# Optimization experiments

Hardware: AMD Instinct MI355X
Metric: run time of the kernel (lower is better)

Reference implementation:

```python
import jax, jax.numpy as jnp
import numpy as np

TEMP = 0.1
NEG = -1e30  # stands in for removing the diagonal via masked_select
EPS = 1e-12  # F.normalize eps


def _l2norm(x, axis):
    n = jnp.linalg.norm(x, axis=axis, keepdims=True)
    return x / jnp.maximum(n, EPS)


def setup_inputs() -> dict:
    key = jax.random.key(0)
    k = jax.random.split(key, 6)
    B, D = 8192, 128      # instance batch, embed dim
    Bp, P = 256, 256      # patch batch, patches per sample
    v1_ins = jax.random.normal(k[0], (B, D), jnp.float32)
    v2_ins = jax.random.normal(k[1], (B, D), jnp.float32)
    v1_patch = jax.random.normal(k[2], (Bp, D, P), jnp.float32)
    v2_patch = jax.random.normal(k[3], (Bp, D, P), jnp.float32)
    v1_counts = jax.random.randint(k[4], (Bp, P), 0, 50, dtype=jnp.int32)
    v2_counts = jax.random.randint(k[5], (Bp, P), 0, 50, dtype=jnp.int32)
    return {"v1_ins": v1_ins, "v2_ins": v2_ins,
            "v1_patch": v1_patch, "v2_patch": v2_patch,
            "v1_counts": v1_counts, "v2_counts": v2_counts}


def _instance_ce(v1, v2):
    B = v1.shape[0]
    embs = jnp.concatenate([_l2norm(v1, 1), _l2norm(v2, 1)], axis=0)  # [2B, D]
    logits = (embs @ embs.T) / TEMP                                    # [2B, 2B]
    N = 2 * B
    # masking the diagonal to -inf == masked_select removal; positive of row i
    # is column (i+B) mod 2B (matches labels after diagonal removal shift)
    logits = jnp.where(jnp.eye(N, dtype=bool), NEG, logits)
    labels = jnp.concatenate([jnp.arange(B) + B, jnp.arange(B)])
    logp = jax.nn.log_softmax(logits, axis=1)
    return -jnp.mean(logp[jnp.arange(N), labels])


def _patch_ce(v1, v2, c1, c2):
    Bp, D, P = v1.shape
    embs = jnp.concatenate([_l2norm(v1, 1), _l2norm(v2, 1)], axis=2)   # [Bp, D, 2P]
    logits = jnp.einsum('bdi,bdj->bij', embs, embs) / TEMP             # [Bp, 2P, 2P]
    N = 2 * P
    logits = jnp.where(jnp.eye(N, dtype=bool)[None], NEG, logits)
    labels = jnp.concatenate([jnp.arange(P) + P, jnp.arange(P)])       # [2P]
    valid = ~jnp.concatenate([c1 == 0, c2 == 0], axis=1)               # [Bp, 2P]
    logp = jax.nn.log_softmax(logits, axis=2)
    pos = logp[:, jnp.arange(N), labels]                               # [Bp, 2P]
    # ignore_index=-100 -> mean over non-ignored elements
    n_valid = jnp.sum(valid.astype(logits.dtype))
    return -jnp.sum(jnp.where(valid, pos, 0.0)) / n_valid


def reference(v1_ins, v2_ins, v1_patch, v2_patch, v1_counts, v2_counts):
    ins_ce = _instance_ce(v1_ins, v2_ins)
    patch_ce = _patch_ce(v1_patch, v2_patch, v1_counts, v2_counts)
    return ins_ce + patch_ce
```

## Files before the change

### kernel.cpp

```cpp
#include <hip/hip_runtime.h>
#include <math.h>

typedef __bf16 bf16_t;
typedef __bf16 bf16x8 __attribute__((ext_vector_type(8)));
typedef float f32x4 __attribute__((ext_vector_type(4)));
typedef float f32x2 __attribute__((ext_vector_type(2)));

#define B_INS 8192
#define N_INS 16384
#define D 128
#define BP 256
#define P 256
#define NP 512

#define C1_CONST 14.426950408889634f

#define WS_ACC 0
#define WS_S 8
#define WS_POS (8 + 16384)
#define WS_SP (8 + 2 * 16384)
#define WS_PP (WS_SP + BP * NP)
#define WS_ZERO_FLOATS (WS_PP + BP * NP)
#define EMB_I_BYTE ((((WS_ZERO_FLOATS) * 4 + 15) / 16) * 16)
#define EMB_P_BYTE (EMB_I_BYTE + N_INS * D * 2)


#define NB_NORMI 128
#define NB_NORMP 2048
#define NB_ZERO 289
#define NB_PREP (NB_NORMI + NB_NORMP + NB_ZERO)
#define NB_INS 1088
#define NB_PATCHB 1024
#define NB_GRAM (NB_INS + NB_PATCHB)
#define NB_FIN 576

__device__ __forceinline__ void load_lds16(const bf16_t* g, bf16_t* l) {
    __builtin_amdgcn_global_load_lds(
        (const __attribute__((address_space(1))) void*)g,
        (__attribute__((address_space(3))) void*)l, 16, 0, 0);
}

__device__ __forceinline__ void stage_panel(const bf16_t* __restrict__ src,
                                            bf16_t* dst, int w, int lane) {
    const bf16_t* g = src + w * 4096 + lane * 8;
    bf16_t* d = dst + w * 4096;
#pragma unroll
    for (int it = 0; it < 8; it++)
        load_lds16(g + it * 512, d + it * 512);
}

__device__ __forceinline__ void load_afrags(const bf16_t* __restrict__ abase,
                                            int rh, int tx, int q, bf16x8 af[4][4]) {
    const bf16_t* a = abase + ((rh * 64 + tx) << 3);
#pragma unroll
    for (int rt = 0; rt < 4; rt++)
#pragma unroll
        for (int ks = 0; ks < 4; ks++)
            af[rt][ks] = *(const bf16x8*)(a + (((ks << 2) + q) << 10) + (rt << 7));
}

__global__ __launch_bounds__(256) void prep_k(const float* __restrict__ v1i,
                                              const float* __restrict__ v2i,
                                              const float* __restrict__ v1p,
                                              const float* __restrict__ v2p,
                                              bf16_t* __restrict__ embI,
                                              bf16_t* __restrict__ embP,
                                              float* __restrict__ ws) {
    __shared__ float L[128][65];
    __shared__ float ps[4][64];
    __shared__ float invs[128];
    int bx = blockIdx.x;
    int t = threadIdx.x;
    if (bx < NB_NORMI) {
        int p = bx;
        const float* srcP = (p < 64) ? (v1i + (size_t)p * 128 * D)
                                     : (v2i + (size_t)(p - 64) * 128 * D);
        {
            int r = t >> 1, h = t & 1;
            const float* row = srcP + (size_t)r * D + h * 64;
            float ss = 0.f;
#pragma unroll
            for (int j = 0; j < 16; j++) {
                float4 v = *(const float4*)(row + j * 4);
                ss += v.x * v.x + v.y * v.y + v.z * v.z + v.w * v.w;
            }
            ss += __shfl_xor(ss, 1, 64);
            if (h == 0) invs[r] = 1.0f / fmaxf(sqrtf(ss), 1e-12f);
        }
        __syncthreads();
#pragma unroll
        for (int it = 0; it < 8; it++) {
            int idx = it * 256 + t;
            int r = idx & 127, g = idx >> 7;
            const float* src8 = srcP + (size_t)r * D + g * 8;
            float4 a = *(const float4*)(src8);
            float4 b = *(const float4*)(src8 + 4);
            float inv = invs[r];
            bf16x8 v;
            v[0] = (bf16_t)(a.x * inv); v[1] = (bf16_t)(a.y * inv);
            v[2] = (bf16_t)(a.z * inv); v[3] = (bf16_t)(a.w * inv);
            v[4] = (bf16_t)(b.x * inv); v[5] = (bf16_t)(b.y * inv);
            v[6] = (bf16_t)(b.z * inv); v[7] = (bf16_t)(b.w * inv);
            *(bf16x8*)(embI + ((size_t)p << 14) + (g << 10) + (r << 3)) = v;
        }
    } else if (bx < NB_NORMI + NB_NORMP) {
        int bx2 = bx - NB_NORMI;
        int b = bx2 >> 3, h = (bx2 >> 2) & 1, chunk = bx2 & 3;
        int i0 = chunk * 64;
        const float* src = ((h == 0) ? v1p : v2p) + (size_t)b * D * P;
#pragma unroll
        for (int it = 0; it < 8; it++) {
            int fi = it * 256 + t;
            int d = fi >> 4, c4 = fi & 15;
            float4 v = *(const float4*)(src + (size_t)d * P + i0 + c4 * 4);
            L[d][c4 * 4 + 0] = v.x;
            L[d][c4 * 4 + 1] = v.y;
            L[d][c4 * 4 + 2] = v.z;
            L[d][c4 * 4 + 3] = v.w;
        }
        __syncthreads();
        {
            int col = t & 63, part = t >> 6;
            float ss = 0.f;
#pragma unroll 8
            for (int d = part * 32; d < part * 32 + 32; d++) { float x = L[d][col]; ss += x * x; }
            ps[part][col] = ss;
        }
        __syncthreads();
        if (t < 64) {
            float n2 = ps[0][t] + ps[1][t] + ps[2][t] + ps[3][t];
            invs[t] = 1.0f / fmaxf(sqrtf(n2), 1e-12f);
        }
        __syncthreads();
#pragma unroll
        for (int it = 0; it < 4; it++) {
            int idx = it * 256 + t;
            int ic = idx & 63, g = idx >> 6;
            float inv = invs[ic];
            bf16x8 v;
#pragma unroll
            for (int j = 0; j < 8; j++) v[j] = (bf16_t)(L[g * 8 + j][ic] * inv);
            int iLoc = h * P + i0 + ic;
            *(bf16x8*)(embP + ((size_t)b << 16) + ((size_t)(iLoc >> 7) << 14) +
                       (g << 10) + ((iLoc & 127) << 3)) = v;
        }
    } else {
        int idx = (bx - NB_NORMI - NB_NORMP) * 256 + t;
        if (idx < WS_ZERO_FLOATS / 4)
            ((f32x4*)ws)[idx] = (f32x4){0.f, 0.f, 0.f, 0.f};
    }
}

__global__ __launch_bounds__(256) void gram_k(const bf16_t* __restrict__ embI,
                                              const bf16_t* __restrict__ embP,
                                              float* __restrict__ S,
                                              float* __restrict__ pos,
                                              float* __restrict__ Sp,
                                              float* __restrict__ posp) {
    __shared__ __align__(16) bf16_t shB[2][16384];
    int t = threadIdx.x, w = t >> 6, lane = t & 63;
    int tx = lane & 15, q = lane >> 4;
    int rh = w & 1, ch = w >> 1;
    int bx = blockIdx.x;

    const bf16_t *Abase, *Bbase;
    float *Sarr, *posArr;
    int R, c0, n, diagC, posC;
    if (bx < NB_INS) {
        int bid = bx, k = 0, cum = 0;
        while (bid >= cum + 8 * (16 - k)) { cum += 8 * (16 - k); k++; }
        int rem = bid - cum, cc = 16 - k;
        R = 8 * k + rem / cc;
        int ci = rem - (rem / cc) * cc;
        c0 = R + ci * 8;
        n = min(8, 128 - c0);
        Abase = embI + ((size_t)R << 14);
        Bbase = embI;
        Sarr = S; posArr = pos;
        diagC = R; posC = R + 64;
    } else {
        int pi = bx - NB_INS;
        int b = pi >> 2; R = pi & 3;
        c0 = R; n = 4 - R;
        const bf16_t* base = embP + ((size_t)b << 16);
        Abase = base + ((size_t)R << 14);
        Bbase = base;
        Sarr = Sp + (size_t)b * NP; posArr = posp + (size_t)b * NP;
        diagC = R; posC = R + 2;
    }
    int rowBase = R * 128;

    bf16x8 af[4][4];
    load_afrags(Abase, rh, tx, q, af);

    f32x2 rowS2[8];
#pragma unroll
    for (int i = 0; i < 8; i++) rowS2[i] = (f32x2){0.f, 0.f};

    stage_panel(Bbase + ((size_t)c0 << 14), shB[0], w, lane);
    int cur = 0;
    for (int ti = 0; ti < n; ti++) {
        int C = c0 + ti;
        __syncthreads();
        if (ti + 1 < n)
            stage_panel(Bbase + ((size_t)(C + 1) << 14), shB[cur ^ 1], w, lane);
        bool isDiag = (C == diagC), isPos = (C == posC);
        int colBase = C * 128;
        const bf16_t* sb = shB[cur];

        float colS[4];
#pragma unroll
        for (int nt = 0; nt < 4; nt++) {
            bf16x8 bf[4];
#pragma unroll
            for (int ks = 0; ks < 4; ks++)
                bf[ks] = *(const bf16x8*)(sb + (((ks << 2) + q) << 10) +
                                          ((ch * 64 + nt * 16 + tx) << 3));
            f32x4 acc[4];
#pragma unroll
            for (int rt = 0; rt < 4; rt++) acc[rt] = (f32x4){0.f, 0.f, 0.f, 0.f};
#pragma unroll
            for (int ks = 0; ks < 4; ks++)
#pragma unroll
                for (int rt = 0; rt < 4; rt++)
                    acc[rt] = __builtin_amdgcn_mfma_f32_16x16x32_bf16(
                        af[rt][ks], bf[ks], acc[rt], 0, 0, 0);

            f32x2 cs = (f32x2){0.f, 0.f};
#pragma unroll
            for (int rt = 0; rt < 4; rt++) {
                f32x2 l0 = {acc[rt][0], acc[rt][1]};
                f32x2 l1 = {acc[rt][2], acc[rt][3]};
                l0 = l0 * C1_CONST - C1_CONST;
                l1 = l1 * C1_CONST - C1_CONST;
                f32x2 e0 = {__builtin_amdgcn_exp2f(l0.x), __builtin_amdgcn_exp2f(l0.y)};
                f32x2 e1 = {__builtin_amdgcn_exp2f(l1.x), __builtin_amdgcn_exp2f(l1.y)};
                if (isDiag) {
                    int inRow = rh * 64 + rt * 16 + q * 4;
                    int inCol = ch * 64 + nt * 16 + tx;
                    if (inRow + 0 == inCol) e0.x = 0.f;
                    if (inRow + 1 == inCol) e0.y = 0.f;
                    if (inRow + 2 == inCol) e1.x = 0.f;
                    if (inRow + 3 == inCol) e1.y = 0.f;
                }
                rowS2[rt * 2] += e0;
                rowS2[rt * 2 + 1] += e1;
                cs += e0 + e1;
            }
            colS[nt] = cs.x + cs.y;

            if (isPos && ch == rh) {
                int reg = tx - q * 4;
                if (reg >= 0 && reg < 4) {
                    float pl = acc[nt][reg] * 10.0f;
                    atomicAdd(&posArr[rowBase + rh * 64 + nt * 16 + tx], pl);
                    atomicAdd(&posArr[colBase + rh * 64 + nt * 16 + tx], pl);
                }
            }
        }
        if (!isDiag) {
#pragma unroll
            for (int i = 0; i < 4; i++) {
                colS[i] += __shfl_xor(colS[i], 16, 64);
                colS[i] += __shfl_xor(colS[i], 32, 64);
            }
            if (q == 0) {
#pragma unroll
                for (int nt = 0; nt < 4; nt++)
                    atomicAdd(&Sarr[colBase + ch * 64 + nt * 16 + tx], colS[nt]);
            }
        }
        cur ^= 1;
    }
    float* rowS = (float*)rowS2;
#pragma unroll
    for (int off = 1; off <= 8; off <<= 1)
#pragma unroll
        for (int i = 0; i < 16; i++) rowS[i] += __shfl_xor(rowS[i], off, 16);
    if (tx == 0) {
#pragma unroll
        for (int rt = 0; rt < 4; rt++)
#pragma unroll
            for (int reg = 0; reg < 4; reg++)
                atomicAdd(&Sarr[rowBase + rh * 64 + rt * 16 + q * 4 + reg],
                          rowS[rt * 4 + reg]);
    }
}

__global__ __launch_bounds__(256) void fin_k(const float* __restrict__ S,
                                             const float* __restrict__ pos,
                                             const float* __restrict__ Sp,
                                             const float* __restrict__ posp,
                                             const int* __restrict__ c1,
                                             const int* __restrict__ c2,
                                             float* __restrict__ acc,
                                             float* __restrict__ out) {
    int bx = blockIdx.x, t = threadIdx.x;
    int lane = t & 63, w = t >> 6;
    float va = 0.f, nv = 0.f;
    if (bx < 64) {
        int i = bx * 256 + t;
        va = __logf(S[i]) + 10.0f - pos[i];
    } else {
        int idx = (bx - 64) * 256 + t;
        int b = idx >> 9, i = idx & 511;
        int cnt = (i < P) ? c1[b * P + i] : c2[b * P + i - P];
        bool valid = (cnt != 0);
        va = valid ? (__logf(Sp[idx]) + 10.0f - posp[idx]) : 0.f;
        nv = valid ? 1.0f : 0.0f;
    }
#pragma unroll
    for (int off = 32; off >= 1; off >>= 1) {
        va += __shfl_down(va, off, 64);
        nv += __shfl_down(nv, off, 64);
    }
    __shared__ float ps[4], pn[4];
    if (lane == 0) { ps[w] = va; pn[w] = nv; }
    __syncthreads();
    if (t == 0) {
        float sv = ps[0] + ps[1] + ps[2] + ps[3];
        float sn = pn[0] + pn[1] + pn[2] + pn[3];
        if (bx < 64) {
            atomicAdd(&acc[0], sv);
        } else {
            atomicAdd(&acc[1], sv);
            atomicAdd(&acc[2], sn);
        }
        __threadfence();
        unsigned old = atomicAdd((unsigned*)&acc[3], 1u);
        if (old == NB_FIN - 1) {
            float a0 = atomicAdd(&acc[0], 0.0f);
            float a1 = atomicAdd(&acc[1], 0.0f);
            float a2 = atomicAdd(&acc[2], 0.0f);
            out[0] = a0 * (1.0f / (float)N_INS) + a1 / a2;
        }
    }
}

extern "C" void kernel_launch(void* const* d_in, const int* in_sizes, int n_in,
                              void* d_out, int out_size, void* d_ws, size_t ws_size,
                              hipStream_t stream) {
    const float* v1i = (const float*)d_in[0];
    const float* v2i = (const float*)d_in[1];
    const float* v1p = (const float*)d_in[2];
    const float* v2p = (const float*)d_in[3];
    const int* c1 = (const int*)d_in[4];
    const int* c2 = (const int*)d_in[5];
    float* ws = (float*)d_ws;
    float* out = (float*)d_out;
    bf16_t* embI = (bf16_t*)((char*)d_ws + EMB_I_BYTE);
    bf16_t* embP = (bf16_t*)((char*)d_ws + EMB_P_BYTE);

    prep_k<<<NB_PREP, 256, 0, stream>>>(v1i, v2i, v1p, v2p, embI, embP, ws);
    gram_k<<<NB_GRAM, 256, 0, stream>>>(embI, embP, ws + WS_S, ws + WS_POS,
                                        ws + WS_SP, ws + WS_PP);
    fin_k<<<NB_FIN, 256, 0, stream>>>(ws + WS_S, ws + WS_POS, ws + WS_SP,
                                      ws + WS_PP, c1, c2, ws + WS_ACC, out);
}
```

Measured before the change: 221.9 us.

## Stage half-width 64-column B panels in gram kernel and parallelize instance normalization

The gram kernel now stages 64-column halves of each B panel, so the double buffer in LDS shrinks to half its size and the pipeline runs twice as many smaller iterations. Diagonal, positive-pair and column-sum indexing are remapped to the 64-column granularity. Separately, instance-row normalization now uses 256 blocks with four threads per row, each holding its 32 floats in registers, which removes the second pass over global memory. The smaller LDS footprint may raise occupancy, at the cost of more barriers and more column atomics per row tile.

After: 232.2 us. 4.7% more time.

```diff
diff --git a/kernel.cpp b/kernel.cpp
--- a/kernel.cpp
+++ b/kernel.cpp
@@ -25,7 +25,7 @@
 #define EMB_P_BYTE (EMB_I_BYTE + N_INS * D * 2)
 
 
-#define NB_NORMI 128
+#define NB_NORMI 256
 #define NB_NORMP 2048
 #define NB_ZERO 289
 #define NB_PREP (NB_NORMI + NB_NORMP + NB_ZERO)
@@ -40,13 +40,14 @@
         (__attribute__((address_space(3))) void*)l, 16, 0, 0);
 }
 
-__device__ __forceinline__ void stage_panel(const bf16_t* __restrict__ src,
-                                            bf16_t* dst, int w, int lane) {
-    const bf16_t* g = src + w * 4096 + lane * 8;
-    bf16_t* d = dst + w * 4096;
-#pragma unroll
-    for (int it = 0; it < 8; it++)
-        load_lds16(g + it * 512, d + it * 512);
+__device__ __forceinline__ void stage_half(const bf16_t* __restrict__ panel,
+                                           int c0loc, bf16_t* dst, int w, int lane) {
+    const bf16_t* g = panel + ((c0loc + lane) << 3);
+#pragma unroll
+    for (int it = 0; it < 4; it++) {
+        int gi = w * 4 + it;
+        load_lds16(g + (gi << 10), dst + (gi << 9));
+    }
 }
 
 __device__ __forceinline__ void load_afrags(const bf16_t* __restrict__ abase,
@@ -68,40 +69,34 @@
                                               float* __restrict__ ws) {
     __shared__ float L[128][65];
     __shared__ float ps[4][64];
-    __shared__ float invs[128];
+    __shared__ float invs[64];
     int bx = blockIdx.x;
     int t = threadIdx.x;
     if (bx < NB_NORMI) {
-        int p = bx;
-        const float* srcP = (p < 64) ? (v1i + (size_t)p * 128 * D)
-                                     : (v2i + (size_t)(p - 64) * 128 * D);
-        {
-            int r = t >> 1, h = t & 1;
-            const float* row = srcP + (size_t)r * D + h * 64;
-            float ss = 0.f;
-#pragma unroll
-            for (int j = 0; j < 16; j++) {
-                float4 v = *(const float4*)(row + j * 4);
-                ss += v.x * v.x + v.y * v.y + v.z * v.z + v.w * v.w;
-            }
-            ss += __shfl_xor(ss, 1, 64);
-            if (h == 0) invs[r] = 1.0f / fmaxf(sqrtf(ss), 1e-12f);
-        }
-        __syncthreads();
-#pragma unroll
-        for (int it = 0; it < 8; it++) {
-            int idx = it * 256 + t;
-            int r = idx & 127, g = idx >> 7;
-            const float* src8 = srcP + (size_t)r * D + g * 8;
-            float4 a = *(const float4*)(src8);
-            float4 b = *(const float4*)(src8 + 4);
-            float inv = invs[r];
+        int r = t >> 2, h = t & 3;
+        int i = bx * 64 + r;
+        const float* row = ((i < B_INS) ? (v1i + (size_t)i * D)
+                                        : (v2i + (size_t)(i - B_INS) * D)) + h * 32;
+        float4 f[8];
+#pragma unroll
+        for (int j = 0; j < 8; j++) f[j] = *(const float4*)(row + j * 4);
+        float ss = 0.f;
+#pragma unroll
+        for (int j = 0; j < 8; j++)
+            ss += f[j].x * f[j].x + f[j].y * f[j].y + f[j].z * f[j].z + f[j].w * f[j].w;
+        ss += __shfl_xor(ss, 1, 64);
+        ss += __shfl_xor(ss, 2, 64);
+        float inv = 1.0f / fmaxf(sqrtf(ss), 1e-12f);
+        int p = i >> 7, rl = i & 127;
+#pragma unroll
+        for (int j = 0; j < 4; j++) {
+            float4 a = f[2 * j], b = f[2 * j + 1];
             bf16x8 v;
             v[0] = (bf16_t)(a.x * inv); v[1] = (bf16_t)(a.y * inv);
             v[2] = (bf16_t)(a.z * inv); v[3] = (bf16_t)(a.w * inv);
             v[4] = (bf16_t)(b.x * inv); v[5] = (bf16_t)(b.y * inv);
             v[6] = (bf16_t)(b.z * inv); v[7] = (bf16_t)(b.w * inv);
-            *(bf16x8*)(embI + ((size_t)p << 14) + (g << 10) + (r << 3)) = v;
+            *(bf16x8*)(embI + ((size_t)p << 14) + ((h * 4 + j) << 10) + (rl << 3)) = v;
         }
     } else if (bx < NB_NORMI + NB_NORMP) {
         int bx2 = bx - NB_NORMI;
@@ -157,36 +152,36 @@
                                               float* __restrict__ pos,
                                               float* __restrict__ Sp,
                                               float* __restrict__ posp) {
-    __shared__ __align__(16) bf16_t shB[2][16384];
+    __shared__ __align__(16) bf16_t shB[2][8192];
     int t = threadIdx.x, w = t >> 6, lane = t & 63;
     int tx = lane & 15, q = lane >> 4;
-    int rh = w & 1, ch = w >> 1;
+    int rh = w & 1, cq = w >> 1;
     int bx = blockIdx.x;
 
     const bf16_t *Abase, *Bbase;
     float *Sarr, *posArr;
-    int R, c0, n, diagC, posC;
+    int R, c0, n, diag0, pos0;
     if (bx < NB_INS) {
         int bid = bx, k = 0, cum = 0;
         while (bid >= cum + 8 * (16 - k)) { cum += 8 * (16 - k); k++; }
         int rem = bid - cum, cc = 16 - k;
         R = 8 * k + rem / cc;
         int ci = rem - (rem / cc) * cc;
-        c0 = R + ci * 8;
-        n = min(8, 128 - c0);
+        c0 = 2 * R + ci * 16;
+        n = min(16, 256 - c0);
         Abase = embI + ((size_t)R << 14);
         Bbase = embI;
         Sarr = S; posArr = pos;
-        diagC = R; posC = R + 64;
+        diag0 = 2 * R; pos0 = 2 * R + 128;
     } else {
         int pi = bx - NB_INS;
         int b = pi >> 2; R = pi & 3;
-        c0 = R; n = 4 - R;
+        c0 = 2 * R; n = 8 - 2 * R;
         const bf16_t* base = embP + ((size_t)b << 16);
         Abase = base + ((size_t)R << 14);
         Bbase = base;
         Sarr = Sp + (size_t)b * NP; posArr = posp + (size_t)b * NP;
-        diagC = R; posC = R + 2;
+        diag0 = 2 * R; pos0 = 2 * R + 4;
     }
     int rowBase = R * 128;
 
@@ -197,25 +192,30 @@
 #pragma unroll
     for (int i = 0; i < 8; i++) rowS2[i] = (f32x2){0.f, 0.f};
 
-    stage_panel(Bbase + ((size_t)c0 << 14), shB[0], w, lane);
+    stage_half(Bbase + ((size_t)(c0 >> 1) << 14), (c0 & 1) * 64, shB[0], w, lane);
     int cur = 0;
     for (int ti = 0; ti < n; ti++) {
-        int C = c0 + ti;
+        int C64 = c0 + ti;
         __syncthreads();
-        if (ti + 1 < n)
-            stage_panel(Bbase + ((size_t)(C + 1) << 14), shB[cur ^ 1], w, lane);
-        bool isDiag = (C == diagC), isPos = (C == posC);
-        int colBase = C * 128;
+        if (ti + 1 < n) {
+            int nc = C64 + 1;
+            stage_half(Bbase + ((size_t)(nc >> 1) << 14), (nc & 1) * 64,
+                       shB[cur ^ 1], w, lane);
+        }
+        int h = C64 & 1;
+        bool isDiag = ((C64 & ~1) == diag0);
+        bool isPos = ((C64 & ~1) == pos0);
+        int colBase = C64 * 64;
         const bf16_t* sb = shB[cur];
 
-        float colS[4];
-#pragma unroll
-        for (int nt = 0; nt < 4; nt++) {
+        float colS[2];
+#pragma unroll
+        for (int nt = 0; nt < 2; nt++) {
+            int cloc = cq * 32 + nt * 16 + tx;
             bf16x8 bf[4];
 #pragma unroll
             for (int ks = 0; ks < 4; ks++)
-                bf[ks] = *(const bf16x8*)(sb + (((ks << 2) + q) << 10) +
-                                          ((ch * 64 + nt * 16 + tx) << 3));
+                bf[ks] = *(const bf16x8*)(sb + (((ks << 2) + q) << 9) + (cloc << 3));
             f32x4 acc[4];
 #pragma unroll
             for (int rt = 0; rt < 4; rt++) acc[rt] = (f32x4){0.f, 0.f, 0.f, 0.f};
@@ -235,13 +235,12 @@
                 l1 = l1 * C1_CONST - C1_CONST;
                 f32x2 e0 = {__builtin_amdgcn_exp2f(l0.x), __builtin_amdgcn_exp2f(l0.y)};
                 f32x2 e1 = {__builtin_amdgcn_exp2f(l1.x), __builtin_amdgcn_exp2f(l1.y)};
-                if (isDiag) {
-                    int inRow = rh * 64 + rt * 16 + q * 4;
-                    int inCol = ch * 64 + nt * 16 + tx;
-                    if (inRow + 0 == inCol) e0.x = 0.f;
-                    if (inRow + 1 == inCol) e0.y = 0.f;
-                    if (inRow + 2 == inCol) e1.x = 0.f;
-                    if (inRow + 3 == inCol) e1.y = 0.f;
+                if (isDiag && rh == h) {
+                    int inRow = rt * 16 + q * 4;
+                    if (inRow + 0 == cloc) e0.x = 0.f;
+                    if (inRow + 1 == cloc) e0.y = 0.f;
+                    if (inRow + 2 == cloc) e1.x = 0.f;
+                    if (inRow + 3 == cloc) e1.y = 0.f;
                 }
                 rowS2[rt * 2] += e0;
                 rowS2[rt * 2 + 1] += e1;
@@ -249,25 +248,26 @@
             }
             colS[nt] = cs.x + cs.y;
 
-            if (isPos && ch == rh) {
+            if (isPos && rh == h) {
                 int reg = tx - q * 4;
                 if (reg >= 0 && reg < 4) {
-                    float pl = acc[nt][reg] * 10.0f;
-                    atomicAdd(&posArr[rowBase + rh * 64 + nt * 16 + tx], pl);
-                    atomicAdd(&posArr[colBase + rh * 64 + nt * 16 + tx], pl);
+                    int rt_m = cq * 2 + nt;
+                    float pl = acc[rt_m][reg] * 10.0f;
+                    atomicAdd(&posArr[rowBase + rh * 64 + rt_m * 16 + tx], pl);
+                    atomicAdd(&posArr[colBase + cloc], pl);
                 }
             }
         }
         if (!isDiag) {
 #pragma unroll
-            for (int i = 0; i < 4; i++) {
+            for (int i = 0; i < 2; i++) {
                 colS[i] += __shfl_xor(colS[i], 16, 64);
                 colS[i] += __shfl_xor(colS[i], 32, 64);
             }
             if (q == 0) {
 #pragma unroll
-                for (int nt = 0; nt < 4; nt++)
-                    atomicAdd(&Sarr[colBase + ch * 64 + nt * 16 + tx], colS[nt]);
+                for (int nt = 0; nt < 2; nt++)
+                    atomicAdd(&Sarr[colBase + cq * 32 + nt * 16 + tx], colS[nt]);
             }
         }
         cur ^= 1;
```

## Load Gram B-fragments directly from global into registers, drop LDS staging

Applied to the files above, without the earlier changes.

The Gram kernel no longer stages 128-column B panels into shared memory with global_load_lds and per-panel barriers. Each wave now loads its B fragments straight from global memory into two register buffers, prefetching two steps ahead. The instance strip length shrinks from 8 to 4 panels, roughly doubling the number of instance blocks for more parallelism. The instance normalization is also reworked so one quad of threads owns a row and keeps it in registers, over twice as many blocks. The aim is to remove LDS traffic and sync overhead, at the cost of redundant global or L2 reads across waves and more atomics from the extra strips.

After: 247.9 us. +11.7%, slower.

```diff
diff --git a/kernel.cpp b/kernel.cpp
--- a/kernel.cpp
+++ b/kernel.cpp
@@ -25,29 +25,14 @@
 #define EMB_P_BYTE (EMB_I_BYTE + N_INS * D * 2)
 
 
-#define NB_NORMI 128
+#define NB_NORMI 256
 #define NB_NORMP 2048
 #define NB_ZERO 289
 #define NB_PREP (NB_NORMI + NB_NORMP + NB_ZERO)
-#define NB_INS 1088
+#define NB_INS 2112
 #define NB_PATCHB 1024
 #define NB_GRAM (NB_INS + NB_PATCHB)
 #define NB_FIN 576
-
-__device__ __forceinline__ void load_lds16(const bf16_t* g, bf16_t* l) {
-    __builtin_amdgcn_global_load_lds(
-        (const __attribute__((address_space(1))) void*)g,
-        (__attribute__((address_space(3))) void*)l, 16, 0, 0);
-}
-
-__device__ __forceinline__ void stage_panel(const bf16_t* __restrict__ src,
-                                            bf16_t* dst, int w, int lane) {
-    const bf16_t* g = src + w * 4096 + lane * 8;
-    bf16_t* d = dst + w * 4096;
-#pragma unroll
-    for (int it = 0; it < 8; it++)
-        load_lds16(g + it * 512, d + it * 512);
-}
 
 __device__ __forceinline__ void load_afrags(const bf16_t* __restrict__ abase,
                                             int rh, int tx, int q, bf16x8 af[4][4]) {
@@ -68,40 +53,34 @@
                                               float* __restrict__ ws) {
     __shared__ float L[128][65];
     __shared__ float ps[4][64];
-    __shared__ float invs[128];
+    __shared__ float invs[64];
     int bx = blockIdx.x;
     int t = threadIdx.x;
     if (bx < NB_NORMI) {
-        int p = bx;
-        const float* srcP = (p < 64) ? (v1i + (size_t)p * 128 * D)
-                                     : (v2i + (size_t)(p - 64) * 128 * D);
-        {
-            int r = t >> 1, h = t & 1;
-            const float* row = srcP + (size_t)r * D + h * 64;
-            float ss = 0.f;
-#pragma unroll
-            for (int j = 0; j < 16; j++) {
-                float4 v = *(const float4*)(row + j * 4);
-                ss += v.x * v.x + v.y * v.y + v.z * v.z + v.w * v.w;
-            }
-            ss += __shfl_xor(ss, 1, 64);
-            if (h == 0) invs[r] = 1.0f / fmaxf(sqrtf(ss), 1e-12f);
-        }
-        __syncthreads();
-#pragma unroll
-        for (int it = 0; it < 8; it++) {
-            int idx = it * 256 + t;
-            int r = idx & 127, g = idx >> 7;
-            const float* src8 = srcP + (size_t)r * D + g * 8;
-            float4 a = *(const float4*)(src8);
-            float4 b = *(const float4*)(src8 + 4);
-            float inv = invs[r];
+        int r = t >> 2, h = t & 3;
+        int i = bx * 64 + r;
+        const float* row = ((i < B_INS) ? (v1i + (size_t)i * D)
+                                        : (v2i + (size_t)(i - B_INS) * D)) + h * 32;
+        float4 f[8];
+#pragma unroll
+        for (int j = 0; j < 8; j++) f[j] = *(const float4*)(row + j * 4);
+        float ss = 0.f;
+#pragma unroll
+        for (int j = 0; j < 8; j++)
+            ss += f[j].x * f[j].x + f[j].y * f[j].y + f[j].z * f[j].z + f[j].w * f[j].w;
+        ss += __shfl_xor(ss, 1, 64);
+        ss += __shfl_xor(ss, 2, 64);
+        float inv = 1.0f / fmaxf(sqrtf(ss), 1e-12f);
+        int p = i >> 7, rl = i & 127;
+#pragma unroll
+        for (int j = 0; j < 4; j++) {
+            float4 a = f[2 * j], b = f[2 * j + 1];
             bf16x8 v;
             v[0] = (bf16_t)(a.x * inv); v[1] = (bf16_t)(a.y * inv);
             v[2] = (bf16_t)(a.z * inv); v[3] = (bf16_t)(a.w * inv);
             v[4] = (bf16_t)(b.x * inv); v[5] = (bf16_t)(b.y * inv);
             v[6] = (bf16_t)(b.z * inv); v[7] = (bf16_t)(b.w * inv);
-            *(bf16x8*)(embI + ((size_t)p << 14) + (g << 10) + (r << 3)) = v;
+            *(bf16x8*)(embI + ((size_t)p << 14) + ((h * 4 + j) << 10) + (rl << 3)) = v;
         }
     } else if (bx < NB_NORMI + NB_NORMP) {
         int bx2 = bx - NB_NORMI;
@@ -151,13 +130,83 @@
     }
 }
 
+__device__ __forceinline__ void gram_step(int it, int itn, int c0, int coff,
+                                          const bf16_t* __restrict__ Bbase,
+                                          bf16x8 (&bufC)[4],
+                                          const bf16x8 (&af)[4][4],
+                                          int diagC, int posC, int rowBase,
+                                          int rh, int ch, int tx, int q,
+                                          f32x2 (&rowS2)[8],
+                                          float* __restrict__ Sarr,
+                                          float* __restrict__ posArr) {
+    int ti = it >> 2, nt = it & 3;
+    int C = c0 + ti;
+    bool isDiag = (C == diagC), isPos = (C == posC);
+    int colBase = C * 128;
+
+    f32x4 acc[4];
+#pragma unroll
+    for (int rt = 0; rt < 4; rt++) acc[rt] = (f32x4){0.f, 0.f, 0.f, 0.f};
+#pragma unroll
+    for (int ks = 0; ks < 4; ks++)
+#pragma unroll
+        for (int rt = 0; rt < 4; rt++)
+            acc[rt] = __builtin_amdgcn_mfma_f32_16x16x32_bf16(
+                af[rt][ks], bufC[ks], acc[rt], 0, 0, 0);
+
+    if (it + 2 < itn) {
+        int i2 = it + 2;
+        const bf16_t* bb = Bbase + ((size_t)(c0 + (i2 >> 2)) << 14) + coff +
+                           ((i2 & 3) << 7);
+#pragma unroll
+        for (int ks = 0; ks < 4; ks++)
+            bufC[ks] = *(const bf16x8*)(bb + (((ks << 2) + q) << 10));
+    }
+
+    f32x2 cs = (f32x2){0.f, 0.f};
+#pragma unroll
+    for (int rt = 0; rt < 4; rt++) {
+        f32x2 l0 = {acc[rt][0], acc[rt][1]};
+        f32x2 l1 = {acc[rt][2], acc[rt][3]};
+        l0 = l0 * C1_CONST - C1_CONST;
+        l1 = l1 * C1_CONST - C1_CONST;
+        f32x2 e0 = {__builtin_amdgcn_exp2f(l0.x), __builtin_amdgcn_exp2f(l0.y)};
+        f32x2 e1 = {__builtin_amdgcn_exp2f(l1.x), __builtin_amdgcn_exp2f(l1.y)};
+        if (isDiag) {
+            int inRow = rh * 64 + rt * 16 + q * 4;
+            int inCol = ch * 64 + nt * 16 + tx;
+            if (inRow + 0 == inCol) e0.x = 0.f;
+            if (inRow + 1 == inCol) e0.y = 0.f;
+            if (inRow + 2 == inCol) e1.x = 0.f;
+            if (inRow + 3 == inCol) e1.y = 0.f;
+        }
+        rowS2[rt * 2] += e0;
+        rowS2[rt * 2 + 1] += e1;
+        cs += e0 + e1;
+    }
+    float colS = cs.x + cs.y;
+    if (!isDiag) {
+        colS += __shfl_xor(colS, 16, 64);
+        colS += __shfl_xor(colS, 32, 64);
+        if (q == 0)
+            atomicAdd(&Sarr[colBase + ch * 64 + nt * 16 + tx], colS);
+    }
+    if (isPos && ch == rh) {
+        int reg = tx - q * 4;
+        if (reg >= 0 && reg < 4) {
+            float pl = acc[nt][reg] * 10.0f;
+            atomicAdd(&posArr[rowBase + rh * 64 + nt * 16 + tx], pl);
+            atomicAdd(&posArr[colBase + ch * 64 + nt * 16 + tx], pl);
+        }
+    }
+}
+
 __global__ __launch_bounds__(256) void gram_k(const bf16_t* __restrict__ embI,
                                               const bf16_t* __restrict__ embP,
                                               float* __restrict__ S,
                                               float* __restrict__ pos,
                                               float* __restrict__ Sp,
                                               float* __restrict__ posp) {
-    __shared__ __align__(16) bf16_t shB[2][16384];
     int t = threadIdx.x, w = t >> 6, lane = t & 63;
     int tx = lane & 15, q = lane >> 4;
     int rh = w & 1, ch = w >> 1;
@@ -168,12 +217,12 @@
     int R, c0, n, diagC, posC;
     if (bx < NB_INS) {
         int bid = bx, k = 0, cum = 0;
-        while (bid >= cum + 8 * (16 - k)) { cum += 8 * (16 - k); k++; }
-        int rem = bid - cum, cc = 16 - k;
-        R = 8 * k + rem / cc;
+        while (bid >= cum + 4 * (32 - k)) { cum += 4 * (32 - k); k++; }
+        int rem = bid - cum, cc = 32 - k;
+        R = 4 * k + rem / cc;
         int ci = rem - (rem / cc) * cc;
-        c0 = R + ci * 8;
-        n = min(8, 128 - c0);
+        c0 = R + ci * 4;
+        n = min(4, 128 - c0);
         Abase = embI + ((size_t)R << 14);
         Bbase = embI;
         Sarr = S; posArr = pos;
@@ -189,6 +238,7 @@
         diagC = R; posC = R + 2;
     }
     int rowBase = R * 128;
+    int coff = (ch * 64 + tx) << 3;
 
     bf16x8 af[4][4];
     load_afrags(Abase, rh, tx, q, af);
@@ -197,80 +247,22 @@
 #pragma unroll
     for (int i = 0; i < 8; i++) rowS2[i] = (f32x2){0.f, 0.f};
 
-    stage_panel(Bbase + ((size_t)c0 << 14), shB[0], w, lane);
-    int cur = 0;
-    for (int ti = 0; ti < n; ti++) {
-        int C = c0 + ti;
-        __syncthreads();
-        if (ti + 1 < n)
-            stage_panel(Bbase + ((size_t)(C + 1) << 14), shB[cur ^ 1], w, lane);
-        bool isDiag = (C == diagC), isPos = (C == posC);
-        int colBase = C * 128;
-        const bf16_t* sb = shB[cur];
-
-        float colS[4];
-#pragma unroll
-        for (int nt = 0; nt < 4; nt++) {
-            bf16x8 bf[4];
-#pragma unroll
-            for (int ks = 0; ks < 4; ks++)
-                bf[ks] = *(const bf16x8*)(sb + (((ks << 2) + q) << 10) +
-                                          ((ch * 64 + nt * 16 + tx) << 3));
-            f32x4 acc[4];
-#pragma unroll
-            for (int rt = 0; rt < 4; rt++) acc[rt] = (f32x4){0.f, 0.f, 0.f, 0.f};
-#pragma unroll
-            for (int ks = 0; ks < 4; ks++)
-#pragma unroll
-                for (int rt = 0; rt < 4; rt++)
-                    acc[rt] = __builtin_amdgcn_mfma_f32_16x16x32_bf16(
-                        af[rt][ks], bf[ks], acc[rt], 0, 0, 0);
-
-            f32x2 cs = (f32x2){0.f, 0.f};
-#pragma unroll
-            for (int rt = 0; rt < 4; rt++) {
-                f32x2 l0 = {acc[rt][0], acc[rt][1]};
-                f32x2 l1 = {acc[rt][2], acc[rt][3]};
-                l0 = l0 * C1_CONST - C1_CONST;
-                l1 = l1 * C1_CONST - C1_CONST;
-                f32x2 e0 = {__builtin_amdgcn_exp2f(l0.x), __builtin_amdgcn_exp2f(l0.y)};
-                f32x2 e1 = {__builtin_amdgcn_exp2f(l1.x), __builtin_amdgcn_exp2f(l1.y)};
-                if (isDiag) {
-                    int inRow = rh * 64 + rt * 16 + q * 4;
-                    int inCol = ch * 64 + nt * 16 + tx;
-                    if (inRow + 0 == inCol) e0.x = 0.f;
-                    if (inRow + 1 == inCol) e0.y = 0.f;
-                    if (inRow + 2 == inCol) e1.x = 0.f;
-                    if (inRow + 3 == inCol) e1.y = 0.f;
-                }
-                rowS2[rt * 2] += e0;
-                rowS2[rt * 2 + 1] += e1;
-                cs += e0 + e1;
-            }
-            colS[nt] = cs.x + cs.y;
-
-            if (isPos && ch == rh) {
-                int reg = tx - q * 4;
-                if (reg >= 0 && reg < 4) {
-                    float pl = acc[nt][reg] * 10.0f;
-                    atomicAdd(&posArr[rowBase + rh * 64 + nt * 16 + tx], pl);
-                    atomicAdd(&posArr[colBase + rh * 64 + nt * 16 + tx], pl);
-                }
-            }
-        }
-        if (!isDiag) {
-#pragma unroll
-            for (int i = 0; i < 4; i++) {
-                colS[i] += __shfl_xor(colS[i], 16, 64);
-                colS[i] += __shfl_xor(colS[i], 32, 64);
-            }
-            if (q == 0) {
-#pragma unroll
-                for (int nt = 0; nt < 4; nt++)
-                    atomicAdd(&Sarr[colBase + ch * 64 + nt * 16 + tx], colS[nt]);
-            }
-        }
-        cur ^= 1;
+    int itn = n * 4;
+    bf16x8 bufA[4], bufB[4];
+    {
+        const bf16_t* bb0 = Bbase + ((size_t)c0 << 14) + coff;
+#pragma unroll
+        for (int ks = 0; ks < 4; ks++)
+            bufA[ks] = *(const bf16x8*)(bb0 + (((ks << 2) + q) << 10));
+#pragma unroll
+        for (int ks = 0; ks < 4; ks++)
+            bufB[ks] = *(const bf16x8*)(bb0 + (((ks << 2) + q) << 10) + 128);
+    }
+    for (int it = 0; it < itn; it += 2) {
+        gram_step(it, itn, c0, coff, Bbase, bufA, af, diagC, posC, rowBase,
+                  rh, ch, tx, q, rowS2, Sarr, posArr);
+        gram_step(it + 1, itn, c0, coff, Bbase, bufB, af, diagC, posC, rowBase,
+                  rh, ch, tx, q, rowS2, Sarr, posArr);
     }
     float* rowS = (float*)rowS2;
 #pragma unroll
```
